# Kernel tuning notes

Measured on AMD Instinct MI355X. Metric: run time of the kernel, lower is better.

Reference implementation:

```python
import jax, jax.numpy as jnp
import numpy as np

B, T, D, H = 4, 1024, 1024, 16
HD = D // H
MAX_LEN = 1024


def _layernorm(x, g, b, eps=1e-5):
    mu = jnp.mean(x, axis=-1, keepdims=True)
    var = jnp.var(x, axis=-1, keepdims=True)
    return (x - mu) * jax.lax.rsqrt(var + eps) * g + b


def setup_inputs() -> dict:
    key = jax.random.key(0)
    ks = jax.random.split(key, 12)
    s = 1.0 / np.sqrt(D)
    return {
        "src": jax.random.normal(ks[0], (B, T, D), jnp.float32),
        "Wqkv": jax.random.uniform(ks[1], (D, 3 * D), jnp.float32, -s, s),
        "bqkv": jnp.zeros((3 * D,), jnp.float32),
        "Wo": jax.random.uniform(ks[2], (D, D), jnp.float32, -s, s),
        "bo": jnp.zeros((D,), jnp.float32),
        "rel_bias": 0.02 * jax.random.normal(ks[3], (H, 2 * MAX_LEN - 1), jnp.float32),
        "temperature": jnp.float32(1.0),
        "W1": jax.random.uniform(ks[4], (D, 4 * D), jnp.float32, -s, s),
        "b1": jnp.zeros((4 * D,), jnp.float32),
        "W2": jax.random.uniform(ks[5], (4 * D, D), jnp.float32, -1.0 / np.sqrt(4 * D), 1.0 / np.sqrt(4 * D)),
        "b2": jnp.zeros((D,), jnp.float32),
        "ff_scale": jnp.ones((1,), jnp.float32),
        "gamma1": jnp.ones((D,), jnp.float32),
        "beta1": jnp.zeros((D,), jnp.float32),
        "gamma2": jnp.ones((D,), jnp.float32),
        "beta2": jnp.zeros((D,), jnp.float32),
    }


def reference(src, Wqkv, bqkv, Wo, bo, rel_bias, temperature, W1, b1, W2, b2,
              ff_scale, gamma1, beta1, gamma2, beta2):
    b, t, c = src.shape
    # QKV projection -> [3, B, H, T, HD]
    qkv = (src @ Wqkv + bqkv).reshape(b, t, 3, H, HD).transpose(2, 0, 3, 1, 4)
    q, k, v = qkv[0], qkv[1], qkv[2]
    temp = jnp.maximum(temperature, 0.01)  # clamp(min=0.01)
    logits = jnp.einsum("bhqd,bhkd->bhqk", q, k) / temp
    # relative position bias gather: [H, T, T]
    pos = jnp.arange(t)
    rel = pos[None, :] - pos[:, None] + (t - 1)
    logits = logits + rel_bias[:, rel][None]
    attn_weights = jax.nn.softmax(logits, axis=-1)
    attn_out = jnp.einsum("bhqk,bhkd->bhqd", attn_weights, v)
    attn_out = attn_out.transpose(0, 2, 1, 3).reshape(b, t, c) @ Wo + bo
    x = _layernorm(src + attn_out, gamma1, beta1)
    ff = jax.nn.gelu(x @ W1 + b1, approximate=False) @ W2 + b2
    out = _layernorm(x + ff_scale * ff, gamma2, beta2)
    return (out, attn_weights)
```

## Files before the change

### kernel.cpp

```cpp
#include <hip/hip_runtime.h>
#include <math.h>

#define BB 4
#define TT 1024
#define DM 1024
#define NH 16
#define HD 64
#define DFF 4096
#define N3 3072

typedef unsigned short u16;
typedef __attribute__((ext_vector_type(4))) float f32x4;
typedef __attribute__((ext_vector_type(8))) short s16x8;

__device__ __forceinline__ u16 f2bf(float f) {
    union { float f; unsigned u; } v; v.f = f;
    unsigned u = v.u;
    u += 0x7fffu + ((u >> 16) & 1u);
    return (u16)(u >> 16);
}
__device__ __forceinline__ float bf2f(u16 h) {
    union { unsigned u; float f; } v; v.u = ((unsigned)h) << 16;
    return v.f;
}

__device__ __forceinline__ void async_copy16(const void* g, void* l) {
    __builtin_amdgcn_global_load_lds(
        (const __attribute__((address_space(1))) unsigned int*)g,
        (__attribute__((address_space(3))) unsigned int*)l, 16, 0, 0);
}

__global__ __launch_bounds__(256) void cvt_kernel(const float* __restrict__ in,
                                                  u16* __restrict__ out, int n) {
    int i = (blockIdx.x * 256 + threadIdx.x) * 4;
    if (i + 3 < n) {
        out[i + 0] = f2bf(in[i + 0]);
        out[i + 1] = f2bf(in[i + 1]);
        out[i + 2] = f2bf(in[i + 2]);
        out[i + 3] = f2bf(in[i + 3]);
    }
}

template<int TIN>
__global__ __launch_bounds__(256) void transpose_kernel(const void* __restrict__ inv,
                                                        u16* __restrict__ out, int R, int C) {
    __shared__ float tile[32][33];
    const float* inF = (const float*)inv;
    const u16* inH = (const u16*)inv;
    size_t boff = (size_t)blockIdx.z * R * C;
    int c0 = blockIdx.x * 32, r0 = blockIdx.y * 32;
    int tx = threadIdx.x & 31, ty = threadIdx.x >> 5;
    for (int i = 0; i < 4; i++) {
        int r = r0 + ty + i * 8, c = c0 + tx;
        float v = (TIN == 0) ? inF[boff + (size_t)r * C + c] : bf2f(inH[boff + (size_t)r * C + c]);
        tile[ty + i * 8][tx] = v;
    }
    __syncthreads();
    for (int i = 0; i < 4; i++) {
        int rr = r0 + tx, cc = c0 + ty + i * 8;
        out[boff + (size_t)cc * R + rr] = f2bf(tile[tx][ty + i * 8]);
    }
}

template<int EPI, int NT>
__global__ __launch_bounds__(512, 2) void gemm256_kernel(const u16* __restrict__ A,
                                                         const u16* __restrict__ BT,
                                                         const float* __restrict__ bias,
                                                         void* __restrict__ out0v,
                                                         u16* __restrict__ out1,
                                                         u16* __restrict__ out2,
                                                         int M, int N, int Kstride) {
    __shared__ u16 As[4][8192];
    __shared__ u16 Bs[4][8192];
    const int tid = threadIdx.x;
    const int lane = tid & 63;
    const int wave = tid >> 6;
    const int quad = lane >> 4;
    const int l15 = lane & 15;
    const int wm = wave >> 2;
    const int wn = wave & 3;
    const int m0 = blockIdx.y * 256;
    const int n0 = blockIdx.x * 256;
    const int koff = blockIdx.z * (NT * 32);

    const int srow = wave * 32 + (lane >> 2);
    const int schunk = ((lane & 3) ^ ((lane >> 2) & 3)) * 8;
    const u16* aG0 = A + (size_t)(m0 + srow) * Kstride + koff + schunk;
    const u16* aG1 = aG0 + (size_t)16 * Kstride;
    const u16* bG0 = BT + (size_t)(n0 + srow) * Kstride + koff + schunk;
    const u16* bG1 = bG0 + (size_t)16 * Kstride;
    const int ldst0 = wave * 1024;
    const int ldst1 = wave * 1024 + 512;

#define STAGE_A(t) { int kk_ = (t) * 32; \
    async_copy16(aG0 + kk_, &As[(t) & 3][ldst0]); \
    async_copy16(aG1 + kk_, &As[(t) & 3][ldst1]); }
#define STAGE_B(t) { int kk_ = (t) * 32; \
    async_copy16(bG0 + kk_, &Bs[(t) & 3][ldst0]); \
    async_copy16(bG1 + kk_, &Bs[(t) & 3][ldst1]); }

    const int swq = (quad ^ (l15 & 3)) * 8;
    const int abase = (wm * 128 + l15) * 32 + swq;
    const int bbase = (wn * 64 + l15) * 32 + swq;

    f32x4 acc[8][4] = {};

    STAGE_A(0); STAGE_B(0);
    STAGE_A(1); STAGE_B(1);
    STAGE_A(2); STAGE_B(2);

#pragma unroll 1
    for (int t = 0; t < NT; ++t) {
        if (t < NT - 2)       asm volatile("s_waitcnt vmcnt(8)" ::: "memory");
        else if (t == NT - 2) asm volatile("s_waitcnt vmcnt(4)" ::: "memory");
        else                  asm volatile("s_waitcnt vmcnt(0)" ::: "memory");
        asm volatile("" ::: "memory");
        __builtin_amdgcn_s_barrier();
        asm volatile("" ::: "memory");

        const u16* as = As[t & 3];
        const u16* bs = Bs[t & 3];

        s16x8 bfr[4];
#pragma unroll
        for (int j = 0; j < 4; j++)
            bfr[j] = *(const s16x8*)&bs[bbase + j * 512];
        s16x8 afr[4];
#pragma unroll
        for (int i = 0; i < 4; i++)
            afr[i] = *(const s16x8*)&as[abase + i * 512];
        if (t + 3 < NT) STAGE_A(t + 3);
        __builtin_amdgcn_s_setprio(1);
#pragma unroll
        for (int i = 0; i < 4; i++)
#pragma unroll
            for (int j = 0; j < 4; j++)
                acc[i][j] = __builtin_amdgcn_mfma_f32_16x16x32_bf16(afr[i], bfr[j], acc[i][j], 0, 0, 0);
        __builtin_amdgcn_s_setprio(0);
#pragma unroll
        for (int i = 0; i < 4; i++)
            afr[i] = *(const s16x8*)&as[abase + 2048 + i * 512];
        if (t + 3 < NT) STAGE_B(t + 3);
        __builtin_amdgcn_s_setprio(1);
#pragma unroll
        for (int i = 0; i < 4; i++)
#pragma unroll
            for (int j = 0; j < 4; j++)
                acc[i + 4][j] = __builtin_amdgcn_mfma_f32_16x16x32_bf16(afr[i], bfr[j], acc[i + 4][j], 0, 0, 0);
        __builtin_amdgcn_s_setprio(0);
    }
#undef STAGE_A
#undef STAGE_B

    const size_t MN = (size_t)M * N;
#pragma unroll
    for (int i = 0; i < 8; i++) {
#pragma unroll
        for (int j = 0; j < 4; j++) {
            f32x4 c = acc[i][j];
            int gn = n0 + wn * 64 + j * 16 + l15;
            float bv = (EPI == 3) ? 0.f : bias[gn];
#pragma unroll
            for (int r = 0; r < 4; r++) {
                int gm = m0 + wm * 128 + i * 16 + quad * 4 + r;
                float v = c[r] + bv;
                if (EPI == 2) {
                    v = 0.5f * v * (1.f + erff(v * 0.70710678118f));
                    ((u16*)out0v)[(size_t)gm * N + gn] = f2bf(v);
                } else if (EPI == 3) {
                    ((float*)out0v)[(size_t)blockIdx.z * MN + (size_t)gm * N + gn] = v;
                } else {
                    int which = gn >> 10, h = (gn >> 6) & 15, d = gn & 63;
                    int bb = gm >> 10, tq = gm & 1023;
                    u16* dst = (which == 0) ? (u16*)out0v : ((which == 1) ? out1 : out2);
                    dst[((size_t)(bb * NH + h) * TT + tq) * HD + d] = f2bf(v);
                }
            }
        }
    }
}

__global__ __launch_bounds__(512) void attn_kernel(const u16* __restrict__ Qb,
                                                   const u16* __restrict__ Kb,
                                                   const u16* __restrict__ VTb,
                                                   const float* __restrict__ rel_bias,
                                                   const float* __restrict__ temp_p,
                                                   float* __restrict__ probs_out,
                                                   u16* __restrict__ attn_out) {
    __shared__ __align__(16) u16 Qs[16 * 72];
    __shared__ __align__(16) u16 Ps[16 * 1032];
    __shared__ float red[2][8][16];
    __shared__ float RB[1040];

    const int tid = threadIdx.x;
    const int lane = tid & 63, wave = tid >> 6, quad = lane >> 4, l15 = lane & 15;
    const int q0 = blockIdx.x * 16;
    const int h = blockIdx.y, b = blockIdx.z;
    const int bh = b * NH + h;
    const size_t headoff = (size_t)bh * TT * HD;

    float temp = fmaxf(temp_p[0], 0.01f);
    const float itemp = 1.f / temp;

    for (int i = tid; i < 1039; i += 512)
        RB[i] = rel_bias[h * 2047 + (1008 - q0) + i];
    if (tid < 256) {
        int row = tid >> 4, col = (tid & 15) * 4;
        const u16* srcp = Qb + headoff + (size_t)(q0 + row) * HD + col;
        *(uint2*)&Qs[row * 72 + col] = *(const uint2*)srcp;
    }
    __syncthreads();

    s16x8 a0 = *(const s16x8*)&Qs[l15 * 72 + quad * 8];
    s16x8 a1 = *(const s16x8*)&Qs[l15 * 72 + 32 + quad * 8];
    f32x4 s[8];
    const u16* Kh = Kb + headoff;
#pragma unroll
    for (int nt = 0; nt < 8; nt++) {
        int key = wave * 128 + nt * 16 + l15;
        const u16* kp = Kh + (size_t)key * HD;
        s16x8 b0 = *(const s16x8*)(kp + quad * 8);
        s16x8 b1 = *(const s16x8*)(kp + 32 + quad * 8);
        f32x4 acc = {};
        acc = __builtin_amdgcn_mfma_f32_16x16x32_bf16(a0, b0, acc, 0, 0, 0);
        acc = __builtin_amdgcn_mfma_f32_16x16x32_bf16(a1, b1, acc, 0, 0, 0);
#pragma unroll
        for (int r = 0; r < 4; r++)
            acc[r] = acc[r] * itemp + RB[key - (quad * 4 + r) + 15];
        s[nt] = acc;
    }

    float lm[4];
#pragma unroll
    for (int r = 0; r < 4; r++) {
        float m = s[0][r];
#pragma unroll
        for (int nt = 1; nt < 8; nt++) m = fmaxf(m, s[nt][r]);
        for (int off = 8; off >= 1; off >>= 1) m = fmaxf(m, __shfl_xor(m, off));
        lm[r] = m;
    }
    if (l15 == 0)
        for (int r = 0; r < 4; r++) red[0][wave][quad * 4 + r] = lm[r];
    __syncthreads();
    float rm[4];
#pragma unroll
    for (int r = 0; r < 4; r++) {
        int row = quad * 4 + r;
        float m = red[0][0][row];
#pragma unroll
        for (int w = 1; w < 8; w++) m = fmaxf(m, red[0][w][row]);
        rm[r] = m;
    }

    float ls[4] = {0.f, 0.f, 0.f, 0.f};
#pragma unroll
    for (int nt = 0; nt < 8; nt++)
#pragma unroll
        for (int r = 0; r < 4; r++) {
            float p = __expf(s[nt][r] - rm[r]);
            s[nt][r] = p;
            ls[r] += p;
        }
#pragma unroll
    for (int r = 0; r < 4; r++) {
        float v = ls[r];
        for (int off = 8; off >= 1; off >>= 1) v += __shfl_xor(v, off);
        ls[r] = v;
    }
    if (l15 == 0)
        for (int r = 0; r < 4; r++) red[1][wave][quad * 4 + r] = ls[r];
    __syncthreads();
    float inv[4];
#pragma unroll
    for (int r = 0; r < 4; r++) {
        int row = quad * 4 + r;
        float v = red[1][0][row];
#pragma unroll
        for (int w = 1; w < 8; w++) v += red[1][w][row];
        inv[r] = 1.f / v;
    }

    float* prow = probs_out + ((size_t)bh * TT + q0) * TT;
#pragma unroll
    for (int nt = 0; nt < 8; nt++) {
        int key = wave * 128 + nt * 16 + l15;
#pragma unroll
        for (int r = 0; r < 4; r++) {
            int row = quad * 4 + r;
            float pn = s[nt][r] * inv[r];
            prow[(size_t)row * TT + key] = pn;
            Ps[row * 1032 + key] = f2bf(pn);
        }
    }
    __syncthreads();

    f32x4 o[4] = {};
    const u16* Vh = VTb + headoff;
#pragma unroll
    for (int ks = 0; ks < 4; ks++) {
        int k0 = wave * 128 + ks * 32;
        s16x8 pa = *(const s16x8*)&Ps[l15 * 1032 + k0 + quad * 8];
#pragma unroll
        for (int nt = 0; nt < 4; nt++) {
            int d = nt * 16 + l15;
            s16x8 vb = *(const s16x8*)(Vh + (size_t)d * TT + k0 + quad * 8);
            o[nt] = __builtin_amdgcn_mfma_f32_16x16x32_bf16(pa, vb, o[nt], 0, 0, 0);
        }
    }
    __syncthreads();
    float* OpF = (float*)Ps;
#pragma unroll
    for (int nt = 0; nt < 4; nt++)
#pragma unroll
        for (int r = 0; r < 4; r++)
            OpF[(wave * 16 + quad * 4 + r) * 64 + nt * 16 + l15] = o[nt][r];
    __syncthreads();

    {
        int m = tid >> 5, dc = (tid & 31) * 2;
        float a0v = 0.f, a1v = 0.f;
#pragma unroll
        for (int w = 0; w < 8; w++) {
            a0v += OpF[(w * 16 + m) * 64 + dc];
            a1v += OpF[(w * 16 + m) * 64 + dc + 1];
        }
        u16 pk[2] = {f2bf(a0v), f2bf(a1v)};
        *(unsigned*)&attn_out[((size_t)(b * TT + q0 + m)) * DM + h * HD + dc] = *(unsigned*)pk;
    }
}

template<int MODE, int KS>
__global__ __launch_bounds__(256) void ln_kernel(const float* __restrict__ af32,
                                                 const u16* __restrict__ abf,
                                                 const float* __restrict__ part,
                                                 const float* __restrict__ biasN,
                                                 const float* __restrict__ scale_p,
                                                 const float* __restrict__ gamma,
                                                 const float* __restrict__ beta,
                                                 float* __restrict__ outf,
                                                 u16* __restrict__ outbf) {
    __shared__ float red[2][4];
    const size_t MN = (size_t)BB * TT * DM;
    int row = blockIdx.x;
    int tid = threadIdx.x;
    float sc = (MODE == 1) ? scale_p[0] : 1.f;
    int c0 = tid * 4;
    size_t base = (size_t)row * DM + c0;
    float4 a = *(const float4*)(biasN + c0);
    float acc[4] = {a.x, a.y, a.z, a.w};
#pragma unroll
    for (int kz = 0; kz < KS; kz++) {
        float4 p = *(const float4*)(part + kz * MN + base);
        acc[0] += p.x; acc[1] += p.y; acc[2] += p.z; acc[3] += p.w;
    }
    float x[4];
#pragma unroll
    for (int c = 0; c < 4; c++) {
        float b0 = (MODE == 0) ? af32[base + c] : bf2f(abf[base + c]);
        x[c] = b0 + sc * acc[c];
    }
    float s = x[0] + x[1] + x[2] + x[3];
    float sq = x[0] * x[0] + x[1] * x[1] + x[2] * x[2] + x[3] * x[3];
    for (int off = 32; off >= 1; off >>= 1) {
        s += __shfl_xor(s, off);
        sq += __shfl_xor(sq, off);
    }
    int wave = tid >> 6;
    if ((tid & 63) == 0) {
        red[0][wave] = s;
        red[1][wave] = sq;
    }
    __syncthreads();
    s = red[0][0] + red[0][1] + red[0][2] + red[0][3];
    sq = red[1][0] + red[1][1] + red[1][2] + red[1][3];
    float mu = s * (1.f / DM);
    float var = sq * (1.f / DM) - mu * mu;
    float rs = rsqrtf(var + 1e-5f);
#pragma unroll
    for (int c = 0; c < 4; c++) {
        float y = (x[c] - mu) * rs * gamma[c0 + c] + beta[c0 + c];
        if (MODE == 0) outbf[base + c] = f2bf(y);
        else outf[base + c] = y;
    }
}

#define OFF_SRCBF 0UL
#define OFF_WQKVT 8388608UL
#define OFF_WOT 14680064UL
#define OFF_W1T 16777216UL
#define OFF_W2T 25165824UL
#define OFF_Q 33554432UL
#define OFF_K 41943040UL
#define OFF_V 50331648UL
#define OFF_VT 58720256UL
#define OFF_ATTNO 67108864UL
#define OFF_XBF 83886080UL
#define OFF_H1 92274688UL
#define OFF_PART 134217728UL

extern "C" void kernel_launch(void* const* d_in, const int* in_sizes, int n_in,
                              void* d_out, int out_size, void* d_ws, size_t ws_size,
                              hipStream_t stream) {
    const float* src = (const float*)d_in[0];
    const float* Wqkv = (const float*)d_in[1];
    const float* bqkv = (const float*)d_in[2];
    const float* Wo = (const float*)d_in[3];
    const float* bo = (const float*)d_in[4];
    const float* relb = (const float*)d_in[5];
    const float* temp = (const float*)d_in[6];
    const float* W1 = (const float*)d_in[7];
    const float* b1 = (const float*)d_in[8];
    const float* W2 = (const float*)d_in[9];
    const float* b2 = (const float*)d_in[10];
    const float* ffs = (const float*)d_in[11];
    const float* g1 = (const float*)d_in[12];
    const float* be1 = (const float*)d_in[13];
    const float* g2 = (const float*)d_in[14];
    const float* be2 = (const float*)d_in[15];

    char* ws = (char*)d_ws;
    u16* srcbf = (u16*)(ws + OFF_SRCBF);
    u16* WqkvT = (u16*)(ws + OFF_WQKVT);
    u16* WoT = (u16*)(ws + OFF_WOT);
    u16* W1T = (u16*)(ws + OFF_W1T);
    u16* W2T = (u16*)(ws + OFF_W2T);
    u16* Qb = (u16*)(ws + OFF_Q);
    u16* Kb = (u16*)(ws + OFF_K);
    u16* Vb = (u16*)(ws + OFF_V);
    u16* VTb = (u16*)(ws + OFF_VT);
    u16* attnbf = (u16*)(ws + OFF_ATTNO);
    u16* xbf = (u16*)(ws + OFF_XBF);
    u16* h1bf = (u16*)(ws + OFF_H1);
    float* partF = (float*)(ws + OFF_PART);

    float* out_f = (float*)d_out;
    float* probs = out_f + (size_t)BB * TT * DM;

    cvt_kernel<<<4096, 256, 0, stream>>>(src, srcbf, BB * TT * DM);
    transpose_kernel<0><<<dim3(N3 / 32, DM / 32, 1), 256, 0, stream>>>(Wqkv, WqkvT, DM, N3);
    transpose_kernel<0><<<dim3(DM / 32, DM / 32, 1), 256, 0, stream>>>(Wo, WoT, DM, DM);
    transpose_kernel<0><<<dim3(DFF / 32, DM / 32, 1), 256, 0, stream>>>(W1, W1T, DM, DFF);
    transpose_kernel<0><<<dim3(DM / 32, DFF / 32, 1), 256, 0, stream>>>(W2, W2T, DFF, DM);
    gemm256_kernel<1, 32><<<dim3(N3 / 256, (BB * TT) / 256, 1), 512, 0, stream>>>(
        srcbf, WqkvT, bqkv, Qb, Kb, Vb, BB * TT, N3, DM);
    transpose_kernel<1><<<dim3(HD / 32, TT / 32, BB * NH), 256, 0, stream>>>(Vb, VTb, TT, HD);
    attn_kernel<<<dim3(TT / 16, NH, BB), 512, 0, stream>>>(Qb, Kb, VTb, relb, temp, probs, attnbf);
    gemm256_kernel<3, 16><<<dim3(DM / 256, (BB * TT) / 256, 2), 512, 0, stream>>>(
        attnbf, WoT, nullptr, partF, nullptr, nullptr, BB * TT, DM, DM);
    ln_kernel<0, 2><<<BB * TT, 256, 0, stream>>>(src, nullptr, partF, bo, nullptr, g1, be1,
                                                 nullptr, xbf);
    gemm256_kernel<2, 32><<<dim3(DFF / 256, (BB * TT) / 256, 1), 512, 0, stream>>>(
        xbf, W1T, b1, h1bf, nullptr, nullptr, BB * TT, DFF, DM);
    gemm256_kernel<3, 32><<<dim3(DM / 256, (BB * TT) / 256, 4), 512, 0, stream>>>(
        h1bf, W2T, nullptr, partF, nullptr, nullptr, BB * TT, DM, DFF);
    ln_kernel<1, 4><<<BB * TT, 256, 0, stream>>>(nullptr, xbf, partF, b2, ffs, g2, be2,
                                                 out_f, nullptr);
}
```

Baseline: 658.6 us.

## Fuse prep kernels, merge softmax reductions, split Wo GEMM four ways

Merges the src fp32-to-bf16 conversion and the four weight transposes into a single prep launch, and vectorises the src conversion. In the attention kernel, the separate block-wide max and sum reductions become one shared-memory round with an online-softmax style rescale, which removes one __syncthreads. The output-projection GEMM now uses a 4-way K split instead of 2-way, with the following layernorm summing four partials. This trades fewer launches and barriers for extra exp work and more partial-sum traffic.

```diff
diff --git a/kernel.cpp b/kernel.cpp
--- a/kernel.cpp
+++ b/kernel.cpp
@@ -30,30 +30,52 @@
         (__attribute__((address_space(3))) unsigned int*)l, 16, 0, 0);
 }
 
-__global__ __launch_bounds__(256) void cvt_kernel(const float* __restrict__ in,
-                                                  u16* __restrict__ out, int n) {
-    int i = (blockIdx.x * 256 + threadIdx.x) * 4;
-    if (i + 3 < n) {
-        out[i + 0] = f2bf(in[i + 0]);
-        out[i + 1] = f2bf(in[i + 1]);
-        out[i + 2] = f2bf(in[i + 2]);
-        out[i + 3] = f2bf(in[i + 3]);
-    }
-}
-
-template<int TIN>
-__global__ __launch_bounds__(256) void transpose_kernel(const void* __restrict__ inv,
-                                                        u16* __restrict__ out, int R, int C) {
+__global__ __launch_bounds__(256) void prep_kernel(const float* __restrict__ src,
+                                                   u16* __restrict__ srcbf,
+                                                   const float* __restrict__ Wqkv,
+                                                   u16* __restrict__ WqkvT,
+                                                   const float* __restrict__ Wo,
+                                                   u16* __restrict__ WoT,
+                                                   const float* __restrict__ W1,
+                                                   u16* __restrict__ W1T,
+                                                   const float* __restrict__ W2,
+                                                   u16* __restrict__ W2T) {
     __shared__ float tile[32][33];
-    const float* inF = (const float*)inv;
-    const u16* inH = (const u16*)inv;
+    int bid = blockIdx.x;
+    int tid = threadIdx.x;
+    if (bid < 4096) {
+        int i = (bid * 256 + tid) * 4;
+        float4 v = *(const float4*)(src + i);
+        u16 pk[4] = {f2bf(v.x), f2bf(v.y), f2bf(v.z), f2bf(v.w)};
+        *(uint2*)(srcbf + i) = *(uint2*)pk;
+        return;
+    }
+    bid -= 4096;
+    const float* in;
+    u16* out;
+    int R, C, bx, by;
+    if (bid < 3072)        { in = Wqkv; out = WqkvT; R = DM;  C = N3;  bx = bid % 96;  by = bid / 96; }
+    else if (bid < 4096)   { bid -= 3072; in = Wo; out = WoT; R = DM;  C = DM;  bx = bid % 32;  by = bid / 32; }
+    else if (bid < 8192)   { bid -= 4096; in = W1; out = W1T; R = DM;  C = DFF; bx = bid % 128; by = bid / 128; }
+    else                   { bid -= 8192; in = W2; out = W2T; R = DFF; C = DM;  bx = bid % 32;  by = bid / 32; }
+    int c0 = bx * 32, r0 = by * 32;
+    int tx = tid & 31, ty = tid >> 5;
+    for (int i = 0; i < 4; i++)
+        tile[ty + i * 8][tx] = in[(size_t)(r0 + ty + i * 8) * C + c0 + tx];
+    __syncthreads();
+    for (int i = 0; i < 4; i++)
+        out[(size_t)(c0 + ty + i * 8) * R + r0 + tx] = f2bf(tile[tx][ty + i * 8]);
+}
+
+__global__ __launch_bounds__(256) void transpose_bf_kernel(const u16* __restrict__ inH,
+                                                           u16* __restrict__ out, int R, int C) {
+    __shared__ float tile[32][33];
     size_t boff = (size_t)blockIdx.z * R * C;
     int c0 = blockIdx.x * 32, r0 = blockIdx.y * 32;
     int tx = threadIdx.x & 31, ty = threadIdx.x >> 5;
     for (int i = 0; i < 4; i++) {
         int r = r0 + ty + i * 8, c = c0 + tx;
-        float v = (TIN == 0) ? inF[boff + (size_t)r * C + c] : bf2f(inH[boff + (size_t)r * C + c]);
-        tile[ty + i * 8][tx] = v;
+        tile[ty + i * 8][tx] = bf2f(inH[boff + (size_t)r * C + c]);
     }
     __syncthreads();
     for (int i = 0; i < 4; i++) {
@@ -239,25 +261,13 @@
         for (int off = 8; off >= 1; off >>= 1) m = fmaxf(m, __shfl_xor(m, off));
         lm[r] = m;
     }
-    if (l15 == 0)
-        for (int r = 0; r < 4; r++) red[0][wave][quad * 4 + r] = lm[r];
-    __syncthreads();
-    float rm[4];
-#pragma unroll
-    for (int r = 0; r < 4; r++) {
-        int row = quad * 4 + r;
-        float m = red[0][0][row];
-#pragma unroll
-        for (int w = 1; w < 8; w++) m = fmaxf(m, red[0][w][row]);
-        rm[r] = m;
-    }
 
     float ls[4] = {0.f, 0.f, 0.f, 0.f};
 #pragma unroll
     for (int nt = 0; nt < 8; nt++)
 #pragma unroll
         for (int r = 0; r < 4; r++) {
-            float p = __expf(s[nt][r] - rm[r]);
+            float p = __expf(s[nt][r] - lm[r]);
             s[nt][r] = p;
             ls[r] += p;
         }
@@ -268,16 +278,24 @@
         ls[r] = v;
     }
     if (l15 == 0)
-        for (int r = 0; r < 4; r++) red[1][wave][quad * 4 + r] = ls[r];
-    __syncthreads();
-    float inv[4];
+#pragma unroll
+        for (int r = 0; r < 4; r++) {
+            red[0][wave][quad * 4 + r] = lm[r];
+            red[1][wave][quad * 4 + r] = ls[r];
+        }
+    __syncthreads();
+
+    float fac[4];
 #pragma unroll
     for (int r = 0; r < 4; r++) {
         int row = quad * 4 + r;
-        float v = red[1][0][row];
-#pragma unroll
-        for (int w = 1; w < 8; w++) v += red[1][w][row];
-        inv[r] = 1.f / v;
+        float M = red[0][0][row];
+#pragma unroll
+        for (int w = 1; w < 8; w++) M = fmaxf(M, red[0][w][row]);
+        float tot = 0.f;
+#pragma unroll
+        for (int w = 0; w < 8; w++) tot += __expf(red[0][w][row] - M) * red[1][w][row];
+        fac[r] = __expf(lm[r] - M) / tot;
     }
 
     float* prow = probs_out + ((size_t)bh * TT + q0) * TT;
@@ -287,7 +305,7 @@
 #pragma unroll
         for (int r = 0; r < 4; r++) {
             int row = quad * 4 + r;
-            float pn = s[nt][r] * inv[r];
+            float pn = s[nt][r] * fac[r];
             prow[(size_t)row * TT + key] = pn;
             Ps[row * 1032 + key] = f2bf(pn);
         }
@@ -436,18 +454,15 @@
     float* out_f = (float*)d_out;
     float* probs = out_f + (size_t)BB * TT * DM;
 
-    cvt_kernel<<<4096, 256, 0, stream>>>(src, srcbf, BB * TT * DM);
-    transpose_kernel<0><<<dim3(N3 / 32, DM / 32, 1), 256, 0, stream>>>(Wqkv, WqkvT, DM, N3);
-    transpose_kernel<0><<<dim3(DM / 32, DM / 32, 1), 256, 0, stream>>>(Wo, WoT, DM, DM);
-    transpose_kernel<0><<<dim3(DFF / 32, DM / 32, 1), 256, 0, stream>>>(W1, W1T, DM, DFF);
-    transpose_kernel<0><<<dim3(DM / 32, DFF / 32, 1), 256, 0, stream>>>(W2, W2T, DFF, DM);
+    prep_kernel<<<16384, 256, 0, stream>>>(src, srcbf, Wqkv, WqkvT, Wo, WoT,
+                                           W1, W1T, W2, W2T);
     gemm256_kernel<1, 32><<<dim3(N3 / 256, (BB * TT) / 256, 1), 512, 0, stream>>>(
         srcbf, WqkvT, bqkv, Qb, Kb, Vb, BB * TT, N3, DM);
-    transpose_kernel<1><<<dim3(HD / 32, TT / 32, BB * NH), 256, 0, stream>>>(Vb, VTb, TT, HD);
+    transpose_bf_kernel<<<dim3(HD / 32, TT / 32, BB * NH), 256, 0, stream>>>(Vb, VTb, TT, HD);
     attn_kernel<<<dim3(TT / 16, NH, BB), 512, 0, stream>>>(Qb, Kb, VTb, relb, temp, probs, attnbf);
-    gemm256_kernel<3, 16><<<dim3(DM / 256, (BB * TT) / 256, 2), 512, 0, stream>>>(
+    gemm256_kernel<3, 8><<<dim3(DM / 256, (BB * TT) / 256, 4), 512, 0, stream>>>(
         attnbf, WoT, nullptr, partF, nullptr, nullptr, BB * TT, DM, DM);
-    ln_kernel<0, 2><<<BB * TT, 256, 0, stream>>>(src, nullptr, partF, bo, nullptr, g1, be1,
+    ln_kernel<0, 4><<<BB * TT, 256, 0, stream>>>(src, nullptr, partF, bo, nullptr, g1, be1,
                                                  nullptr, xbf);
     gemm256_kernel<2, 32><<<dim3(DFF / 256, (BB * TT) / 256, 1), 512, 0, stream>>>(
         xbf, W1T, b1, h1bf, nullptr, nullptr, BB * TT, DFF, DM);
```

Result: no change. 660.8 us (+0.3%).
